# Performance work log

Hardware: AMD Instinct MI355X
Metric: run time of the kernel (lower is better)

The kernel has to match this reference:

```python
import jax, jax.numpy as jnp
import numpy as np

EMBED_DIM = 1024
NUM_HEADS = 16
HEAD_DIM = EMBED_DIM // NUM_HEADS


def setup_inputs() -> dict:
    key = jax.random.key(0)
    k_x, k_wq, k_bq, k_wo, k_bo = jax.random.split(key, 5)
    B, S, E = 4, 2048, EMBED_DIM
    lim_qkv = 1.0 / np.sqrt(E)
    lim_out = 1.0 / np.sqrt(E)
    return {
        "x": jax.random.normal(k_x, (B, S, E), dtype=jnp.float32),
        # nn.Linear stores weight [out, in]; we keep [in, out] for x @ W
        "w_qkv": jax.random.uniform(k_wq, (E, 3 * E), minval=-lim_qkv, maxval=lim_qkv, dtype=jnp.float32),
        "b_qkv": jax.random.uniform(k_bq, (3 * E,), minval=-lim_qkv, maxval=lim_qkv, dtype=jnp.float32),
        "w_out": jax.random.uniform(k_wo, (E, E), minval=-lim_out, maxval=lim_out, dtype=jnp.float32),
        "b_out": jax.random.uniform(k_bo, (E,), minval=-lim_out, maxval=lim_out, dtype=jnp.float32),
    }


def reference(x, w_qkv, b_qkv, w_out, b_out):
    B, S, E = x.shape
    H, D = NUM_HEADS, HEAD_DIM
    qkv = x @ w_qkv + b_qkv                       # [B, S, 3E]
    qkv = qkv.reshape(B, S, H, 3 * D)
    q, k, v = jnp.split(qkv, 3, axis=-1)          # each [B, S, H, D]
    scale = 1.0 / np.sqrt(D).astype(np.float32)
    scores = jnp.einsum("bshd,bthd->bhst", q, k) * scale  # [B, H, S, S]
    attn = jax.nn.softmax(scores, axis=-1)
    out = jnp.einsum("bhst,bthd->bshd", attn, v)  # [B, S, H, D]
    out = out.reshape(B, S, E)
    return out @ w_out + b_out
```

## Files before the change

kernel.cpp:

```cpp
#include <hip/hip_runtime.h>
#include <hip/hip_bf16.h>


typedef short bf16x8 __attribute__((ext_vector_type(8)));
typedef unsigned short u16x8 __attribute__((ext_vector_type(8)));
typedef short s16x4 __attribute__((ext_vector_type(4)));
typedef float f32x4 __attribute__((ext_vector_type(4)));

#define QSCALE 0.18033688011112042f

__device__ inline short f2bf(float f) {
    unsigned int u = __builtin_bit_cast(unsigned int, f);
    u += 0x7fffu + ((u >> 16) & 1u);
    return (short)(u >> 16);
}

__device__ inline unsigned int pack2bf(float a, float b) {
#if __has_builtin(__builtin_amdgcn_cvt_pk_bf16_f32)
    typedef __bf16 bf2 __attribute__((ext_vector_type(2)));
    bf2 v = __builtin_amdgcn_cvt_pk_bf16_f32(a, b);
    return __builtin_bit_cast(unsigned int, v);
#else
    return (unsigned int)(unsigned short)f2bf(a) |
           ((unsigned int)(unsigned short)f2bf(b) << 16);
#endif
}

__device__ inline float fast_exp2(float x) {
#if __has_builtin(__builtin_amdgcn_exp2f)
    return __builtin_amdgcn_exp2f(x);
#else
    float r;
    asm("v_exp_f32 %0, %1" : "=v"(r) : "v"(x));
    return r;
#endif
}

__device__ inline float fast_rcp(float x) {
#if __has_builtin(__builtin_amdgcn_rcpf)
    return __builtin_amdgcn_rcpf(x);
#else
    float r;
    asm("v_rcp_f32 %0, %1" : "=v"(r) : "v"(x));
    return r;
#endif
}

__device__ inline void gload_lds16(const short* g, short* l) {
    __builtin_amdgcn_global_load_lds(
        (const __attribute__((address_space(1))) unsigned int*)g,
        (__attribute__((address_space(3))) unsigned int*)l, 16, 0, 0);
}


__global__ __launch_bounds__(256) void cvt_bf16_kernel(const float* __restrict__ in,
                                                       short* __restrict__ out) {
    int i = blockIdx.x * 256 + threadIdx.x;
    const float4 a = *(const float4*)(in + (size_t)i * 8);
    const float4 b = *(const float4*)(in + (size_t)i * 8 + 4);
    unsigned int o0 = pack2bf(a.x, a.y), o1 = pack2bf(a.z, a.w);
    unsigned int o2 = pack2bf(b.x, b.y), o3 = pack2bf(b.z, b.w);
    uint4 o = {o0, o1, o2, o3};
    *(uint4*)(out + (size_t)i * 8) = o;
}

__global__ __launch_bounds__(256) void transpose_cvt_kernel(const float* __restrict__ in,
                                                            short* __restrict__ out,
                                                            int K, int N) {
    __shared__ float tile[32][33];
    int tx = threadIdx.x & 31, ty = threadIdx.x >> 5;
    int nt = blockIdx.x * 32, kt = blockIdx.y * 32;
    for (int i = 0; i < 4; ++i)
        tile[ty + i * 8][tx] = in[(size_t)(kt + ty + i * 8) * N + nt + tx];
    __syncthreads();
    for (int i = 0; i < 4; ++i)
        out[(size_t)(nt + ty + i * 8) * K + kt + tx] = f2bf(tile[tx][ty + i * 8]);
}

__global__ __launch_bounds__(256, 2) void gemm_qkv_kernel(
        const short* __restrict__ A, const short* __restrict__ Bt,
        const float* __restrict__ bias,
        short* __restrict__ Qg, short* __restrict__ Kg, short* __restrict__ Vtg) {
    __shared__ short As[128 * 64];
    __shared__ short Bs[128 * 64];
    const int t = threadIdx.x;
    const int w = t >> 6, lane = t & 63, r = lane & 15, q4 = lane >> 4;
    const int n0 = blockIdx.x * 128, m0 = blockIdx.y * 128;
    const int wm = (w & 1) * 64, wn = (w >> 1) * 64;

    f32x4 acc[4][4];
    for (int i = 0; i < 4; ++i)
        for (int j = 0; j < 4; ++j)
            acc[i][j] = (f32x4){0.f, 0.f, 0.f, 0.f};

    for (int kk = 0; kk < 1024; kk += 64) {
        for (int ii = 0; ii < 4; ++ii) {
            const int p = t + 256 * ii;
            const int row = p >> 3;
            const int gg = (p & 7) ^ (row & 7);
            gload_lds16(A + (size_t)(m0 + row) * 1024 + kk + gg * 8, &As[p * 8]);
            gload_lds16(Bt + (size_t)(n0 + row) * 1024 + kk + gg * 8, &Bs[p * 8]);
        }
        __syncthreads();
        for (int ko = 0; ko < 2; ++ko) {
            bf16x8 af[4], bfr[4];
            for (int i = 0; i < 4; ++i) {
                const int R = wm + i * 16 + r;
                af[i] = *(const bf16x8*)(&As[R * 64 + (((ko * 4 + q4) ^ (R & 7)) * 8)]);
            }
            for (int j = 0; j < 4; ++j) {
                const int R = wn + j * 16 + r;
                bfr[j] = *(const bf16x8*)(&Bs[R * 64 + (((ko * 4 + q4) ^ (R & 7)) * 8)]);
            }
            for (int i = 0; i < 4; ++i)
                for (int j = 0; j < 4; ++j)
                    acc[i][j] = __builtin_amdgcn_mfma_f32_16x16x32_bf16(af[i], bfr[j], acc[i][j], 0, 0, 0);
        }
        __syncthreads();
    }

    for (int i = 0; i < 4; ++i) {
        for (int j = 0; j < 4; ++j) {
            const int gn = n0 + wn + j * 16 + r;
            const int h = gn / 192;
            const int rr = gn - h * 192;
            const float bv = bias[gn];
            for (int g = 0; g < 4; ++g) {
                const int gm = m0 + wm + i * 16 + q4 * 4 + g;
                const int bb = gm >> 11;
                const int s2 = gm & 2047;
                float v = acc[i][j][g] + bv;
                const size_t bh = (size_t)(bb * 16 + h);
                if (rr < 64) {
                    Qg[(bh * 2048 + s2) * 64 + rr] = f2bf(v * QSCALE);
                } else if (rr < 128) {
                    Kg[(bh * 2048 + s2) * 64 + (rr - 64)] = f2bf(v);
                } else {
                    Vtg[(bh * 64 + (rr - 128)) * 2048 + s2] = f2bf(v);
                }
            }
        }
    }
}

__global__ __launch_bounds__(256, 4) void attn_kernel(
        const short* __restrict__ Qg, const short* __restrict__ Kg,
        const short* __restrict__ Vtg, short* __restrict__ Og) {
    __shared__ short Ks[64 * 64];
    __shared__ short Vs[64 * 64];
    __shared__ short Ps[128 * 64];
    const int t = threadIdx.x;
    const int w = t >> 6, lane = t & 63, r = lane & 15, q4 = lane >> 4;
    const int blk = blockIdx.x;
    const int qt = blk & 15;
    const int h = (blk >> 4) & 15;
    const int b = blk >> 8;
    const size_t bh = (size_t)b * 16 + h;
    const short* Qb = Qg + bh * 2048 * 64;
    const short* Kb = Kg + bh * 2048 * 64;
    const short* Vb = Vtg + bh * 64 * 2048;

    const int r1 = t >> 3, g1 = (t & 7) ^ (r1 & 7);
    const int r2 = 32 + (t >> 3), g2 = (t & 7) ^ (r2 & 7);
    const short* kptr1 = Kb + r1 * 64 + g1 * 8;
    const short* kptr2 = Kb + r2 * 64 + g2 * 8;
    const short* vptr1 = Vb + (size_t)r1 * 2048 + g1 * 8;
    const short* vptr2 = Vb + (size_t)r2 * 2048 + g2 * 8;
    short* klds1 = &Ks[t * 8];
    short* klds2 = &Ks[(256 + t) * 8];
    short* vlds1 = &Vs[t * 8];
    short* vlds2 = &Vs[(256 + t) * 8];

    const int swz = r & 7;
    const int ga = (q4 ^ swz) * 8;
    const int gb = ((4 + q4) ^ swz) * 8;

    bf16x8 qf[2][2];
    for (int qs = 0; qs < 2; ++qs) {
        const int qrow = qt * 128 + w * 32 + qs * 16 + r;
        qf[qs][0] = *(const bf16x8*)(Qb + (size_t)qrow * 64 + q4 * 8);
        qf[qs][1] = *(const bf16x8*)(Qb + (size_t)qrow * 64 + 32 + q4 * 8);
    }

    bf16x8 onesf;
    for (int i = 0; i < 8; ++i) onesf[i] = (short)0x3F80;

    f32x4 o[2][4], ol[2];
    for (int qs = 0; qs < 2; ++qs) {
        ol[qs] = (f32x4){0.f, 0.f, 0.f, 0.f};
        for (int nt = 0; nt < 4; ++nt) o[qs][nt] = (f32x4){0.f, 0.f, 0.f, 0.f};
    }

    const int pbase0 = w * 2048;
    const int pwb = pbase0 + r * 64 + (q4 & 1) * 4;
    const int pgq = q4 >> 1;
    const int prb = pbase0 + r * 64;

    for (int kt = 0; kt < 32; ++kt) {
        gload_lds16(kptr1 + kt * 4096, klds1);
        gload_lds16(kptr2 + kt * 4096, klds2);
        gload_lds16(vptr1 + kt * 64, vlds1);
        gload_lds16(vptr2 + kt * 64, vlds2);
        __syncthreads();

        f32x4 st[2][4];
        for (int c = 0; c < 4; ++c) {
            const int R = (c * 16 + r) * 64;
            const bf16x8 kf0 = *(const bf16x8*)(&Ks[R + ga]);
            const bf16x8 kf1 = *(const bf16x8*)(&Ks[R + gb]);
            for (int qs = 0; qs < 2; ++qs) {
                f32x4 z = (f32x4){0.f, 0.f, 0.f, 0.f};
                z = __builtin_amdgcn_mfma_f32_16x16x32_bf16(kf0, qf[qs][0], z, 0, 0, 0);
                z = __builtin_amdgcn_mfma_f32_16x16x32_bf16(kf1, qf[qs][1], z, 0, 0, 0);
                st[qs][c] = z;
            }
        }

        for (int qs = 0; qs < 2; ++qs) {
            const int pb = pwb + qs * 1024;
            for (int c = 0; c < 4; ++c) {
                const float p0 = fast_exp2(st[qs][c][0]);
                const float p1 = fast_exp2(st[qs][c][1]);
                const float p2 = fast_exp2(st[qs][c][2]);
                const float p3 = fast_exp2(st[qs][c][3]);
                uint2 pk = {pack2bf(p0, p1), pack2bf(p2, p3)};
                *(uint2*)(&Ps[pb + (((c * 2 + pgq) ^ swz) * 8)]) = pk;
            }
        }
        asm volatile("s_waitcnt lgkmcnt(0)" ::: "memory");

        for (int ko = 0; ko < 2; ++ko) {
            const int gk = (ko == 0) ? ga : gb;
            bf16x8 pf[2];
            for (int qs = 0; qs < 2; ++qs)
                pf[qs] = *(const bf16x8*)(&Ps[prb + qs * 1024 + (((ko * 4 + q4) ^ swz) * 8)]);
            for (int qs = 0; qs < 2; ++qs)
                ol[qs] = __builtin_amdgcn_mfma_f32_16x16x32_bf16(onesf, pf[qs], ol[qs], 0, 0, 0);
            for (int nt = 0; nt < 4; ++nt) {
                const bf16x8 vf = *(const bf16x8*)(&Vs[(nt * 16 + r) * 64 + gk]);
                for (int qs = 0; qs < 2; ++qs)
                    o[qs][nt] = __builtin_amdgcn_mfma_f32_16x16x32_bf16(vf, pf[qs], o[qs][nt], 0, 0, 0);
            }
        }
        __syncthreads();
    }

    for (int qs = 0; qs < 2; ++qs) {
        const float inv = fast_rcp(ol[qs][0]);
        const int srow = qt * 128 + w * 32 + qs * 16 + r;
        const size_t base = ((size_t)(b * 2048 + srow)) * 1024 + h * 64;
        for (int nt = 0; nt < 4; ++nt) {
            uint2 pk = {pack2bf(o[qs][nt][0] * inv, o[qs][nt][1] * inv),
                        pack2bf(o[qs][nt][2] * inv, o[qs][nt][3] * inv)};
            *(uint2*)(Og + base + nt * 16 + q4 * 4) = pk;
        }
    }
}

__global__ __launch_bounds__(256, 2) void gemm_out_kernel(
        const short* __restrict__ A, const short* __restrict__ Bt,
        const float* __restrict__ bias, float* __restrict__ out) {
    __shared__ short As[128 * 64];
    __shared__ short Bs[128 * 64];
    const int t = threadIdx.x;
    const int w = t >> 6, lane = t & 63, r = lane & 15, q4 = lane >> 4;
    const int n0 = blockIdx.x * 128, m0 = blockIdx.y * 128;
    const int wm = (w & 1) * 64, wn = (w >> 1) * 64;

    f32x4 acc[4][4];
    for (int i = 0; i < 4; ++i)
        for (int j = 0; j < 4; ++j)
            acc[i][j] = (f32x4){0.f, 0.f, 0.f, 0.f};

    for (int kk = 0; kk < 1024; kk += 64) {
        for (int ii = 0; ii < 4; ++ii) {
            const int p = t + 256 * ii;
            const int row = p >> 3;
            const int gg = (p & 7) ^ (row & 7);
            gload_lds16(A + (size_t)(m0 + row) * 1024 + kk + gg * 8, &As[p * 8]);
            gload_lds16(Bt + (size_t)(n0 + row) * 1024 + kk + gg * 8, &Bs[p * 8]);
        }
        __syncthreads();
        for (int ko = 0; ko < 2; ++ko) {
            bf16x8 af[4], bfr[4];
            for (int i = 0; i < 4; ++i) {
                const int R = wm + i * 16 + r;
                af[i] = *(const bf16x8*)(&As[R * 64 + (((ko * 4 + q4) ^ (R & 7)) * 8)]);
            }
            for (int j = 0; j < 4; ++j) {
                const int R = wn + j * 16 + r;
                bfr[j] = *(const bf16x8*)(&Bs[R * 64 + (((ko * 4 + q4) ^ (R & 7)) * 8)]);
            }
            for (int i = 0; i < 4; ++i)
                for (int j = 0; j < 4; ++j)
                    acc[i][j] = __builtin_amdgcn_mfma_f32_16x16x32_bf16(af[i], bfr[j], acc[i][j], 0, 0, 0);
        }
        __syncthreads();
    }

    for (int i = 0; i < 4; ++i) {
        for (int j = 0; j < 4; ++j) {
            const int gn = n0 + wn + j * 16 + r;
            const float bv = bias[gn];
            for (int g = 0; g < 4; ++g) {
                const int gm = m0 + wm + i * 16 + q4 * 4 + g;
                out[(size_t)gm * 1024 + gn] = acc[i][j][g] + bv;
            }
        }
    }
}


extern "C" void kernel_launch(void* const* d_in, const int* in_sizes, int n_in,
                              void* d_out, int out_size, void* d_ws, size_t ws_size,
                              hipStream_t stream) {
    const float* x     = (const float*)d_in[0];
    const float* w_qkv = (const float*)d_in[1];
    const float* b_qkv = (const float*)d_in[2];
    const float* w_out = (const float*)d_in[3];
    const float* b_out = (const float*)d_in[4];
    float* out = (float*)d_out;

    char* ws = (char*)d_ws;
    short* xb    = (short*)(ws);
    short* wqkvT = (short*)(ws + 16777216);
    short* woutT = (short*)(ws + 23068672);
    short* Qg    = (short*)(ws + 25165824);
    short* Kg    = (short*)(ws + 41943040);
    short* Vtg   = (short*)(ws + 58720256);
    short* attn  = xb;

    cvt_bf16_kernel<<<4096, 256, 0, stream>>>(x, xb);
    transpose_cvt_kernel<<<dim3(96, 32), 256, 0, stream>>>(w_qkv, wqkvT, 1024, 3072);
    transpose_cvt_kernel<<<dim3(32, 32), 256, 0, stream>>>(w_out, woutT, 1024, 1024);
    gemm_qkv_kernel<<<dim3(24, 64), 256, 0, stream>>>(xb, wqkvT, b_qkv, Qg, Kg, Vtg);
    attn_kernel<<<1024, 256, 0, stream>>>(Qg, Kg, Vtg, attn);
    gemm_out_kernel<<<dim3(8, 64), 256, 0, stream>>>(attn, woutT, b_out, out);
}
```

Baseline: 274.4 us.

## Stage V transpose through LDS and give each attention wave 64 query rows

The QKV GEMM epilogue now writes the V part of each tile into shared memory first. It then emits the transposed Vt rows as coalesced 16-byte stores instead of scattered 2-byte strided writes. The attention kernel shrinks to 2 waves of 128 threads, each handling 64 query rows, so every K fragment loaded from LDS is reused across 4 query sub-tiles. Launch bounds drop to 2 blocks per CU. This raises register pressure and halves the threads per block, which risks lower occupancy and less latency hiding.

```diff
diff --git a/kernel.cpp b/kernel.cpp
--- a/kernel.cpp
+++ b/kernel.cpp
@@ -4,7 +4,6 @@
 
 typedef short bf16x8 __attribute__((ext_vector_type(8)));
 typedef unsigned short u16x8 __attribute__((ext_vector_type(8)));
-typedef short s16x4 __attribute__((ext_vector_type(4)));
 typedef float f32x4 __attribute__((ext_vector_type(4)));
 
 #define QSCALE 0.18033688011112042f
@@ -81,8 +80,10 @@
         const short* __restrict__ A, const short* __restrict__ Bt,
         const float* __restrict__ bias,
         short* __restrict__ Qg, short* __restrict__ Kg, short* __restrict__ Vtg) {
-    __shared__ short As[128 * 64];
-    __shared__ short Bs[128 * 64];
+    __shared__ short smem[2 * 128 * 64];
+    short* As = smem;
+    short* Bs = smem + 128 * 64;
+    short* vlds = smem;
     const int t = threadIdx.x;
     const int w = t >> 6, lane = t & 63, r = lane & 15, q4 = lane >> 4;
     const int n0 = blockIdx.x * 128, m0 = blockIdx.y * 128;
@@ -126,7 +127,8 @@
             const int rr = gn - h * 192;
             const float bv = bias[gn];
             for (int g = 0; g < 4; ++g) {
-                const int gm = m0 + wm + i * 16 + q4 * 4 + g;
+                const int sl = wm + i * 16 + q4 * 4 + g;
+                const int gm = m0 + sl;
                 const int bb = gm >> 11;
                 const int s2 = gm & 2047;
                 float v = acc[i][j][g] + bv;
@@ -136,14 +138,28 @@
                 } else if (rr < 128) {
                     Kg[(bh * 2048 + s2) * 64 + (rr - 64)] = f2bf(v);
                 } else {
-                    Vtg[(bh * 64 + (rr - 128)) * 2048 + s2] = f2bf(v);
+                    vlds[(rr - 128) * 130 + sl] = f2bf(v);
                 }
             }
         }
     }
-}
-
-__global__ __launch_bounds__(256, 4) void attn_kernel(
+    __syncthreads();
+    const int xm3 = blockIdx.x % 3;
+    if (xm3 != 0) {
+        const int hv = (xm3 == 1) ? (n0 - 128) / 192 : (n0 - 64) / 192;
+        const size_t bhv = (size_t)((m0 >> 11) * 16 + hv);
+        const int s0 = m0 & 2047;
+        for (int ii = 0; ii < 4; ++ii) {
+            const int gi = t + 256 * ii;
+            const int dd = gi >> 4;
+            const int s8 = (gi & 15) * 8;
+            bf16x8 val = *(const bf16x8*)(&vlds[dd * 130 + s8]);
+            *(bf16x8*)(Vtg + (bhv * 64 + dd) * 2048 + s0 + s8) = val;
+        }
+    }
+}
+
+__global__ __launch_bounds__(128, 2) void attn_kernel(
         const short* __restrict__ Qg, const short* __restrict__ Kg,
         const short* __restrict__ Vtg, short* __restrict__ Og) {
     __shared__ short Ks[64 * 64];
@@ -160,24 +176,28 @@
     const short* Kb = Kg + bh * 2048 * 64;
     const short* Vb = Vtg + bh * 64 * 2048;
 
-    const int r1 = t >> 3, g1 = (t & 7) ^ (r1 & 7);
-    const int r2 = 32 + (t >> 3), g2 = (t & 7) ^ (r2 & 7);
-    const short* kptr1 = Kb + r1 * 64 + g1 * 8;
-    const short* kptr2 = Kb + r2 * 64 + g2 * 8;
-    const short* vptr1 = Vb + (size_t)r1 * 2048 + g1 * 8;
-    const short* vptr2 = Vb + (size_t)r2 * 2048 + g2 * 8;
-    short* klds1 = &Ks[t * 8];
-    short* klds2 = &Ks[(256 + t) * 8];
-    short* vlds1 = &Vs[t * 8];
-    short* vlds2 = &Vs[(256 + t) * 8];
+    const int sr = t >> 3;
+    const int sg = t & 7;
+    const short* kptr[4];
+    const short* vptr[4];
+    short* klds[4];
+    short* vlds_[4];
+    for (int ii = 0; ii < 4; ++ii) {
+        const int row = sr + 16 * ii;
+        const int g = sg ^ (row & 7);
+        kptr[ii] = Kb + row * 64 + g * 8;
+        vptr[ii] = Vb + (size_t)row * 2048 + g * 8;
+        klds[ii] = &Ks[(t + 128 * ii) * 8];
+        vlds_[ii] = &Vs[(t + 128 * ii) * 8];
+    }
 
     const int swz = r & 7;
     const int ga = (q4 ^ swz) * 8;
     const int gb = ((4 + q4) ^ swz) * 8;
 
-    bf16x8 qf[2][2];
-    for (int qs = 0; qs < 2; ++qs) {
-        const int qrow = qt * 128 + w * 32 + qs * 16 + r;
+    bf16x8 qf[4][2];
+    for (int qs = 0; qs < 4; ++qs) {
+        const int qrow = qt * 128 + w * 64 + qs * 16 + r;
         qf[qs][0] = *(const bf16x8*)(Qb + (size_t)qrow * 64 + q4 * 8);
         qf[qs][1] = *(const bf16x8*)(Qb + (size_t)qrow * 64 + 32 + q4 * 8);
     }
@@ -185,44 +205,45 @@
     bf16x8 onesf;
     for (int i = 0; i < 8; ++i) onesf[i] = (short)0x3F80;
 
-    f32x4 o[2][4], ol[2];
-    for (int qs = 0; qs < 2; ++qs) {
+    f32x4 o[4][4], ol[4];
+    for (int qs = 0; qs < 4; ++qs) {
         ol[qs] = (f32x4){0.f, 0.f, 0.f, 0.f};
         for (int nt = 0; nt < 4; ++nt) o[qs][nt] = (f32x4){0.f, 0.f, 0.f, 0.f};
     }
 
-    const int pbase0 = w * 2048;
+    const int pbase0 = w * 4096;
     const int pwb = pbase0 + r * 64 + (q4 & 1) * 4;
     const int pgq = q4 >> 1;
     const int prb = pbase0 + r * 64;
 
     for (int kt = 0; kt < 32; ++kt) {
-        gload_lds16(kptr1 + kt * 4096, klds1);
-        gload_lds16(kptr2 + kt * 4096, klds2);
-        gload_lds16(vptr1 + kt * 64, vlds1);
-        gload_lds16(vptr2 + kt * 64, vlds2);
-        __syncthreads();
-
-        f32x4 st[2][4];
+        for (int ii = 0; ii < 4; ++ii) {
+            gload_lds16(kptr[ii] + kt * 4096, klds[ii]);
+            gload_lds16(vptr[ii] + kt * 64, vlds_[ii]);
+        }
+        __syncthreads();
+
+        bf16x8 kf[4][2];
         for (int c = 0; c < 4; ++c) {
             const int R = (c * 16 + r) * 64;
-            const bf16x8 kf0 = *(const bf16x8*)(&Ks[R + ga]);
-            const bf16x8 kf1 = *(const bf16x8*)(&Ks[R + gb]);
-            for (int qs = 0; qs < 2; ++qs) {
+            kf[c][0] = *(const bf16x8*)(&Ks[R + ga]);
+            kf[c][1] = *(const bf16x8*)(&Ks[R + gb]);
+        }
+
+        for (int qs = 0; qs < 4; ++qs) {
+            f32x4 st[4];
+            for (int c = 0; c < 4; ++c) {
                 f32x4 z = (f32x4){0.f, 0.f, 0.f, 0.f};
-                z = __builtin_amdgcn_mfma_f32_16x16x32_bf16(kf0, qf[qs][0], z, 0, 0, 0);
-                z = __builtin_amdgcn_mfma_f32_16x16x32_bf16(kf1, qf[qs][1], z, 0, 0, 0);
-                st[qs][c] = z;
-            }
-        }
-
-        for (int qs = 0; qs < 2; ++qs) {
+                z = __builtin_amdgcn_mfma_f32_16x16x32_bf16(kf[c][0], qf[qs][0], z, 0, 0, 0);
+                z = __builtin_amdgcn_mfma_f32_16x16x32_bf16(kf[c][1], qf[qs][1], z, 0, 0, 0);
+                st[c] = z;
+            }
             const int pb = pwb + qs * 1024;
             for (int c = 0; c < 4; ++c) {
-                const float p0 = fast_exp2(st[qs][c][0]);
-                const float p1 = fast_exp2(st[qs][c][1]);
-                const float p2 = fast_exp2(st[qs][c][2]);
-                const float p3 = fast_exp2(st[qs][c][3]);
+                const float p0 = fast_exp2(st[c][0]);
+                const float p1 = fast_exp2(st[c][1]);
+                const float p2 = fast_exp2(st[c][2]);
+                const float p3 = fast_exp2(st[c][3]);
                 uint2 pk = {pack2bf(p0, p1), pack2bf(p2, p3)};
                 *(uint2*)(&Ps[pb + (((c * 2 + pgq) ^ swz) * 8)]) = pk;
             }
@@ -231,23 +252,23 @@
 
         for (int ko = 0; ko < 2; ++ko) {
             const int gk = (ko == 0) ? ga : gb;
-            bf16x8 pf[2];
-            for (int qs = 0; qs < 2; ++qs)
+            bf16x8 pf[4];
+            for (int qs = 0; qs < 4; ++qs)
                 pf[qs] = *(const bf16x8*)(&Ps[prb + qs * 1024 + (((ko * 4 + q4) ^ swz) * 8)]);
-            for (int qs = 0; qs < 2; ++qs)
+            for (int qs = 0; qs < 4; ++qs)
                 ol[qs] = __builtin_amdgcn_mfma_f32_16x16x32_bf16(onesf, pf[qs], ol[qs], 0, 0, 0);
             for (int nt = 0; nt < 4; ++nt) {
                 const bf16x8 vf = *(const bf16x8*)(&Vs[(nt * 16 + r) * 64 + gk]);
-                for (int qs = 0; qs < 2; ++qs)
+                for (int qs = 0; qs < 4; ++qs)
                     o[qs][nt] = __builtin_amdgcn_mfma_f32_16x16x32_bf16(vf, pf[qs], o[qs][nt], 0, 0, 0);
             }
         }
         __syncthreads();
     }
 
-    for (int qs = 0; qs < 2; ++qs) {
+    for (int qs = 0; qs < 4; ++qs) {
         const float inv = fast_rcp(ol[qs][0]);
-        const int srow = qt * 128 + w * 32 + qs * 16 + r;
+        const int srow = qt * 128 + w * 64 + qs * 16 + r;
         const size_t base = ((size_t)(b * 2048 + srow)) * 1024 + h * 64;
         for (int nt = 0; nt < 4; ++nt) {
             uint2 pk = {pack2bf(o[qs][nt][0] * inv, o[qs][nt][1] * inv),
@@ -334,6 +355,6 @@
     transpose_cvt_kernel<<<dim3(96, 32), 256, 0, stream>>>(w_qkv, wqkvT, 1024, 3072);
     transpose_cvt_kernel<<<dim3(32, 32), 256, 0, stream>>>(w_out, woutT, 1024, 1024);
     gemm_qkv_kernel<<<dim3(24, 64), 256, 0, stream>>>(xb, wqkvT, b_qkv, Qg, Kg, Vtg);
-    attn_kernel<<<1024, 256, 0, stream>>>(Qg, Kg, Vtg, attn);
+    attn_kernel<<<1024, 128, 0, stream>>>(Qg, Kg, Vtg, attn);
     gemm_out_kernel<<<dim3(8, 64), 256, 0, stream>>>(attn, woutT, b_out, out);
 }
```

Measured after the change: 515.3 us. 1.88x slower.
